# Kernel optimization log

Hardware: AMD Instinct MI355X
Metric: run time of the kernel (lower is better)

Reference implementation:

```python
import jax, jax.numpy as jnp
import numpy as np

B, N, F, T, K, O = 8, 1024, 64, 32, 3, 64


def setup_inputs() -> dict:
    key = jax.random.key(0)
    k0, k1, k2, k3 = jax.random.split(key, 4)
    x = jax.random.normal(k0, (B, N, F, T), dtype=jnp.float32)
    spatial_attention = jax.random.uniform(k1, (B, N, N), dtype=jnp.float32)
    cheb = jax.random.normal(k2, (K, N, N), dtype=jnp.float32) * 0.1  # stacked T_k
    Theta = jax.random.normal(k3, (K, F, O), dtype=jnp.float32) * (1.0 / np.sqrt(F))
    return {"x": x, "spatial_attention": spatial_attention, "cheb": cheb, "Theta": Theta}


def reference(x, spatial_attention, cheb, Theta):
    # Original per-timestep, per-k loop computes:
    #   rhs[b,i,f] = sum_j (T_k[j,i] * att[b,j,i])... note: T_k_with_at.permute(0,2,1) @ x
    #   i.e. rhs[b,i,f,t] = sum_j T_k[j,i]*att[b,j,i]*x[b,j,f,t]
    # Vectorized over all timesteps t and Chebyshev orders k at once.
    rhs = jnp.einsum('kji,bji,bjft->bkift', cheb, spatial_attention, x)  # (B,K,N,F,T)
    out = jnp.einsum('bkift,kfo->biot', rhs, Theta)                      # sum over k,f
    return jax.nn.relu(out)  # (B,N,O,T)
```

## Files before the change

### kernel.cpp

```cpp
#include <hip/hip_runtime.h>
#include <stdint.h>

#define Bn 8
#define Nn 1024
#define Fn 64
#define Tn 32
#define Kn 3
#define On 64
#define Rn (Kn * Nn)
#define Cn (On * Tn)
#define NT (Rn / 64)

typedef __bf16 bf16x8 __attribute__((ext_vector_type(8)));
typedef float f32x4 __attribute__((ext_vector_type(4)));
typedef __attribute__((address_space(1))) void gvoid;
typedef __attribute__((address_space(3))) void lvoid;

union BF8 { bf16x8 v; ushort s[8]; uint4 q; };

static __device__ __forceinline__ ushort f2bf(float f) {
  uint32_t u = __float_as_uint(f);
  return (ushort)((u + 0x7FFFu + ((u >> 16) & 1u)) >> 16);
}

static __device__ __forceinline__ void glds(const ushort* g, ushort* l) {
  __builtin_amdgcn_global_load_lds((gvoid*)g, (lvoid*)l, 16, 0, 0);
}

__global__ void k_thetaT(const float* __restrict__ Theta, ushort* __restrict__ ThT) {
  int idx = blockIdx.x * 256 + threadIdx.x;
  if (idx < Kn * On * Fn) {
    int k = idx / (On * Fn);
    int rem = idx % (On * Fn);
    int o = rem / Fn, f = rem % Fn;
    ThT[idx] = f2bf(Theta[(k * Fn + f) * On + o]);
  }
}

__global__ __launch_bounds__(256) void k_prepW(const float* __restrict__ att,
                                               const float* __restrict__ cheb,
                                               ushort* __restrict__ Wt) {
  __shared__ float tile[32][33];
  int i0 = blockIdx.x * 32, j0 = blockIdx.y * 32;
  int tid = threadIdx.x;
  int ci = tid & 31, rj = tid >> 5;
  float cv[4][Kn];
#pragma unroll
  for (int p = 0; p < 4; p++) {
    int j = j0 + rj + p * 8;
#pragma unroll
    for (int k = 0; k < Kn; k++)
      cv[p][k] = cheb[((size_t)k * Nn + j) * Nn + i0 + ci];
  }
  for (int b = 0; b < Bn; b++) {
    float av[4];
#pragma unroll
    for (int p = 0; p < 4; p++) {
      int j = j0 + rj + p * 8;
      av[p] = att[((size_t)b * Nn + j) * Nn + i0 + ci];
    }
    for (int k = 0; k < Kn; k++) {
#pragma unroll
      for (int p = 0; p < 4; p++)
        tile[rj + p * 8][ci] = av[p] * cv[p][k];
      __syncthreads();
#pragma unroll
      for (int p = 0; p < 4; p++) {
        int i = i0 + rj + p * 8;
        Wt[((size_t)b * Nn + i) * Rn + (size_t)k * Nn + j0 + ci] = f2bf(tile[ci][rj + p * 8]);
      }
      __syncthreads();
    }
  }
}

__global__ __launch_bounds__(512) void k_prepY(const float* __restrict__ x,
                                               const ushort* __restrict__ ThT,
                                               ushort* __restrict__ Yt) {
  __shared__ ushort ylds[1024 * 32];
  int jt = blockIdx.x, b = blockIdx.y;
  int j0 = jt * 32;
  int tid = threadIdx.x;
  int lane = tid & 63, w = tid >> 6;
  int l15 = lane & 15, l4 = lane >> 4;

  BF8 bfr[4][2][2];
#pragma unroll
  for (int jj = 0; jj < 4; jj++) {
    const float* xp = x + ((size_t)b * Nn + (j0 + w * 4 + jj)) * (Fn * Tn);
#pragma unroll
    for (int ks = 0; ks < 2; ks++)
#pragma unroll
      for (int tf = 0; tf < 2; tf++) {
        int t = tf * 16 + l15;
        int fb = ks * 32 + l4 * 8;
#pragma unroll
        for (int e = 0; e < 8; e++)
          bfr[jj][ks][tf].s[e] = f2bf(xp[(fb + e) * Tn + t]);
      }
  }

  for (int k = 0; k < Kn; k++) {
    for (int h = 0; h < 2; h++) {
      BF8 afr[2][2];
#pragma unroll
      for (int o2 = 0; o2 < 2; o2++)
#pragma unroll
        for (int ks = 0; ks < 2; ks++) {
          int o = h * 32 + o2 * 16 + l15;
          afr[o2][ks].q = *(const uint4*)&ThT[((size_t)k * On + o) * Fn + ks * 32 + l4 * 8];
        }
#pragma unroll
      for (int jj = 0; jj < 4; jj++) {
        f32x4 acc[2][2] = {};
#pragma unroll
        for (int ks = 0; ks < 2; ks++)
#pragma unroll
          for (int o2 = 0; o2 < 2; o2++)
#pragma unroll
            for (int tf = 0; tf < 2; tf++)
              acc[o2][tf] = __builtin_amdgcn_mfma_f32_16x16x32_bf16(
                  afr[o2][ks].v, bfr[jj][ks][tf].v, acc[o2][tf], 0, 0, 0);
#pragma unroll
        for (int o2 = 0; o2 < 2; o2++)
#pragma unroll
          for (int tf = 0; tf < 2; tf++)
#pragma unroll
            for (int q = 0; q < 4; q++) {
              int cl = (o2 * 16 + l4 * 4 + q) * Tn + tf * 16 + l15;
              ylds[cl * 32 + w * 4 + jj] = f2bf(acc[o2][tf][q]);
            }
      }
      __syncthreads();
      const uint32_t* yl32 = (const uint32_t*)ylds;
      uint32_t* Yt32 = (uint32_t*)Yt;
      int e = tid & 15, rowst = tid >> 4;
      for (int pass = 0; pass < 32; pass++) {
        int cl = pass * 32 + rowst;
        size_t off = ((size_t)b * Cn + (size_t)(h * 1024 + cl)) * Rn + (size_t)k * Nn + j0;
        Yt32[off / 2 + e] = yl32[cl * 16 + e];
      }
      __syncthreads();
    }
  }
}

__global__ __launch_bounds__(512, 2) void k_gemm(const ushort* __restrict__ Wt,
                                                 const ushort* __restrict__ Yt,
                                                 float* __restrict__ out) {
  extern __shared__ __align__(16) ushort smem[];
  ushort* As = smem;
  ushort* Bs = smem + 32768;

  int g = blockIdx.x;
  int b = g & 7, slot = g >> 3;
  int i0 = (slot & 3) * 256, c0 = (slot >> 2) * 256;
  int tid = threadIdx.x, lane = tid & 63, w = tid >> 6;
  int l15 = lane & 15, l4 = lane >> 4;
  int wm = w >> 2, wn = w & 3;

  const ushort* Ab = Wt + ((size_t)b * Nn + i0) * Rn;
  const ushort* Bb = Yt + ((size_t)b * Cn + c0) * Rn;

  int srcC = (((lane & 7) ^ (lane >> 3)) * 8);
  int arow0 = w * 8 + (lane >> 3);
  int brow0 = (w >> 2) * 64 + (w & 3) * 8 + (lane >> 3);

  int aL = (wm * 64 + l15) * 64;
  int bL = (wn * 32 + l15) * 64;
  int x7 = l15 & 7;
  int colx0 = ((l4) ^ x7) * 8;
  int colx1 = ((4 + l4) ^ x7) * 8;

  f32x4 acc[8][4] = {};
  BF8 afX[4][2], afY[4][2];
  BF8 bfX[2][2], bfY[2][2];

#define MFMA_(a_, b_, c_) __builtin_amdgcn_mfma_f32_16x16x32_bf16((a_), (b_), (c_), 0, 0, 0)
#define BAR() asm volatile("s_barrier" ::: "memory")
#define PRIO1 __builtin_amdgcn_s_setprio(1)
#define PRIO0 __builtin_amdgcn_s_setprio(0)
#define VMC(n_) asm volatile("s_waitcnt vmcnt(" #n_ ")" ::: "memory")

#define STAGE_A(t_, h_) { int bo_ = ((t_) & 1) * 16384 + (h_) * 8192 + w * 512; \
    const ushort* gp_ = Ab + (size_t)(arow0 + (h_) * 64) * Rn + (t_) * 64 + srcC; \
    glds(gp_, As + bo_); \
    glds(gp_ + 128 * (size_t)Rn, As + bo_ + 4096); }
#define STAGE_B(t_, h_) { int bo_ = ((t_) & 1) * 16384 + (h_) * 8192 + w * 512; \
    const ushort* gp_ = Bb + (size_t)(brow0 + (h_) * 32) * Rn + (t_) * 64 + srcC; \
    glds(gp_, Bs + bo_); \
    glds(gp_ + 128 * (size_t)Rn, Bs + bo_ + 4096); }

#define RD_A(DST_, bo_, mh_) { _Pragma("unroll") for (int m = 0; m < 4; m++) { \
    int ba_ = (bo_) + (mh_) * 8192 + aL + m * 1024; \
    DST_[m][0].q = *(const uint4*)&As[ba_ + colx0]; \
    DST_[m][1].q = *(const uint4*)&As[ba_ + colx1]; } }
#define RD_B(DST_, bo_, nh_) { _Pragma("unroll") for (int n = 0; n < 2; n++) { \
    int bb_ = (bo_) + (nh_) * 8192 + bL + n * 1024; \
    DST_[n][0].q = *(const uint4*)&Bs[bb_ + colx0]; \
    DST_[n][1].q = *(const uint4*)&Bs[bb_ + colx1]; } }

#define MMC(AF_, BF_, MO_, NO_) { _Pragma("unroll") for (int ks = 0; ks < 2; ks++) \
    _Pragma("unroll") for (int m = 0; m < 4; m++) \
      _Pragma("unroll") for (int n = 0; n < 2; n++) \
        acc[(MO_) + m][(NO_) + n] = MFMA_(AF_[m][ks].v, BF_[n][ks].v, acc[(MO_) + m][(NO_) + n]); }

  STAGE_A(0, 0); STAGE_B(0, 0); STAGE_B(0, 1); STAGE_A(0, 1); STAGE_A(1, 0);
  VMC(6); BAR();
  RD_A(afX, 0, 0); RD_B(bfX, 0, 0);

#define TILE(t_, S0_, S1_, S2_, W0_, W1_, W3_, LAST_) { \
    int bo_c = ((t_) & 1) * 16384; \
    VMC(W0_); BAR(); \
    RD_B(bfY, bo_c, 1); \
    if (S0_) STAGE_B((t_) + 1, 0); \
    PRIO1; MMC(afX, bfX, 0, 0); PRIO0; \
    VMC(W1_); BAR(); \
    RD_A(afY, bo_c, 1); \
    if (S1_) { STAGE_B((t_) + 1, 1); STAGE_A((t_) + 1, 1); } \
    PRIO1; MMC(afX, bfY, 0, 2); PRIO0; \
    if (S2_) STAGE_A((t_) + 2, 0); \
    PRIO1; MMC(afY, bfX, 4, 0); PRIO0; \
    if (!(LAST_)) { VMC(W3_); BAR(); \
      RD_A(afX, bo_c ^ 16384, 0); RD_B(bfX, bo_c ^ 16384, 0); } \
    PRIO1; MMC(afY, bfY, 4, 2); PRIO0; \
  }

  for (int t = 0; t < NT - 2; ++t)
    TILE(t, 1, 1, 1, 4, 4, 6, 0);
  TILE(NT - 2, 1, 1, 0, 4, 4, 4, 0);
  TILE(NT - 1, 0, 0, 0, 2, 0, 0, 1);

#undef TILE
#undef MMC
#undef RD_B
#undef RD_A
#undef STAGE_B
#undef STAGE_A
#undef VMC

  float* ob = out + (size_t)b * Nn * Cn;
#pragma unroll
  for (int m = 0; m < 8; m++) {
    int i = i0 + wm * 128 + m * 16 + l4 * 4;
#pragma unroll
    for (int n = 0; n < 4; n++) {
      int c = c0 + wn * 64 + n * 16 + l15;
#pragma unroll
      for (int q = 0; q < 4; q++)
        ob[(size_t)(i + q) * Cn + c] = fmaxf(acc[m][n][q], 0.0f);
    }
  }
}

extern "C" void kernel_launch(void* const* d_in, const int* in_sizes, int n_in,
                              void* d_out, int out_size, void* d_ws, size_t ws_size,
                              hipStream_t stream) {
  const float* x     = (const float*)d_in[0];
  const float* att   = (const float*)d_in[1];
  const float* cheb  = (const float*)d_in[2];
  const float* Theta = (const float*)d_in[3];
  float* out = (float*)d_out;

  char* ws = (char*)d_ws;
  ushort* ThT = (ushort*)ws;
  ushort* Wt  = (ushort*)(ws + 65536);
  ushort* Yt  = (ushort*)(ws + 65536 + 50331648ull);

  hipFuncSetAttribute((const void*)k_gemm, hipFuncAttributeMaxDynamicSharedMemorySize, 131072);

  k_thetaT<<<48, 256, 0, stream>>>(Theta, ThT);
  k_prepW<<<dim3(32, 32), 256, 0, stream>>>(att, cheb, Wt);
  k_prepY<<<dim3(32, 8), 512, 0, stream>>>(x, ThT, Yt);
  k_gemm<<<256, 512, 131072, stream>>>(Wt, Yt, out);
}
```

Measured before the change: 155.6 us.

## Restructure GEMM main loop to prefetch full tile two steps ahead

The prologue now loads both halves of A and B for the first two K-tiles before entering the loop. Each loop iteration now issues all global-to-LDS loads for tile t+2, spread across the four MFMA quarters, and uses different vmcnt waits. Next-tile fragment reads from LDS are interleaved between the MFMA blocks so compute overlaps the loads. The aim is to hide global memory latency behind more MFMA work. The cost is more outstanding loads and a more delicate barrier and wait ordering on the double-buffered LDS.

```diff
diff --git a/kernel.cpp b/kernel.cpp
--- a/kernel.cpp
+++ b/kernel.cpp
@@ -205,31 +205,37 @@
       _Pragma("unroll") for (int n = 0; n < 2; n++) \
         acc[(MO_) + m][(NO_) + n] = MFMA_(AF_[m][ks].v, BF_[n][ks].v, acc[(MO_) + m][(NO_) + n]); }
 
-  STAGE_A(0, 0); STAGE_B(0, 0); STAGE_B(0, 1); STAGE_A(0, 1); STAGE_A(1, 0);
-  VMC(6); BAR();
+  STAGE_A(0, 0); STAGE_B(0, 0); STAGE_B(0, 1); STAGE_A(0, 1);
+  STAGE_A(1, 0); STAGE_B(1, 0); STAGE_B(1, 1); STAGE_A(1, 1);
+  VMC(8); BAR();
   RD_A(afX, 0, 0); RD_B(bfX, 0, 0);
 
-#define TILE(t_, S0_, S1_, S2_, W0_, W1_, W3_, LAST_) { \
-    int bo_c = ((t_) & 1) * 16384; \
-    VMC(W0_); BAR(); \
-    RD_B(bfY, bo_c, 1); \
-    if (S0_) STAGE_B((t_) + 1, 0); \
+#define TILE(t_, S2_, W1_, W2_, LAST_) { \
+    int cur = ((t_) & 1) * 16384, nxt = cur ^ 16384; \
+     \
+    RD_B(bfY, cur, 1); \
     PRIO1; MMC(afX, bfX, 0, 0); PRIO0; \
+     \
     VMC(W1_); BAR(); \
-    RD_A(afY, bo_c, 1); \
-    if (S1_) { STAGE_B((t_) + 1, 1); STAGE_A((t_) + 1, 1); } \
+    RD_A(afY, cur, 1); \
+    if (S2_) STAGE_A((t_) + 2, 0); \
     PRIO1; MMC(afX, bfY, 0, 2); PRIO0; \
-    if (S2_) STAGE_A((t_) + 2, 0); \
+    if (!(LAST_)) RD_A(afX, nxt, 0); \
+     \
+    VMC(W2_); BAR(); \
+    if (S2_) { STAGE_B((t_) + 2, 0); STAGE_B((t_) + 2, 1); } \
     PRIO1; MMC(afY, bfX, 4, 0); PRIO0; \
-    if (!(LAST_)) { VMC(W3_); BAR(); \
-      RD_A(afX, bo_c ^ 16384, 0); RD_B(bfX, bo_c ^ 16384, 0); } \
+    if (!(LAST_)) RD_B(bfX, nxt, 0); \
+     \
+    BAR(); \
+    if (S2_) STAGE_A((t_) + 2, 1); \
     PRIO1; MMC(afY, bfY, 4, 2); PRIO0; \
   }
 
   for (int t = 0; t < NT - 2; ++t)
-    TILE(t, 1, 1, 1, 4, 4, 6, 0);
-  TILE(NT - 2, 1, 1, 0, 4, 4, 4, 0);
-  TILE(NT - 1, 0, 0, 0, 2, 0, 0, 1);
+    TILE(t, 1, 6, 4, 0);
+  TILE(NT - 2, 0, 6, 2, 0);
+  TILE(NT - 1, 0, 0, 0, 1);
 
 #undef TILE
 #undef MMC
```

Result: slower. 174.0 us (+11.8%).

## Load GEMM B operand directly from global into registers, drop B LDS staging

Applied to the files above, without the earlier changes.

The B tile (Yt) is no longer staged through LDS; each lane loads its MFMA B fragments straight from global memory into registers, while A keeps the double-buffered LDS path. The pipeline is rewritten as a simpler loop with full vmcnt(0) waits, and dynamic shared memory is halved. This removes LDS traffic and barriers for B, at the cost of duplicated global reads across the waves sharing the same columns and coarser wait synchronisation that can expose latency.

```diff
diff --git a/kernel.cpp b/kernel.cpp
--- a/kernel.cpp
+++ b/kernel.cpp
@@ -150,7 +150,6 @@
                                                  float* __restrict__ out) {
   extern __shared__ __align__(16) ushort smem[];
   ushort* As = smem;
-  ushort* Bs = smem + 32768;
 
   int g = blockIdx.x;
   int b = g & 7, slot = g >> 3;
@@ -164,13 +163,13 @@
 
   int srcC = (((lane & 7) ^ (lane >> 3)) * 8);
   int arow0 = w * 8 + (lane >> 3);
-  int brow0 = (w >> 2) * 64 + (w & 3) * 8 + (lane >> 3);
 
   int aL = (wm * 64 + l15) * 64;
-  int bL = (wn * 32 + l15) * 64;
   int x7 = l15 & 7;
   int colx0 = ((l4) ^ x7) * 8;
   int colx1 = ((4 + l4) ^ x7) * 8;
+
+  const ushort* bG = Bb + (size_t)(wn * 64 + l15) * Rn + l4 * 8;
 
   f32x4 acc[8][4] = {};
   BF8 afX[4][2], afY[4][2];
@@ -180,64 +179,62 @@
 #define BAR() asm volatile("s_barrier" ::: "memory")
 #define PRIO1 __builtin_amdgcn_s_setprio(1)
 #define PRIO0 __builtin_amdgcn_s_setprio(0)
-#define VMC(n_) asm volatile("s_waitcnt vmcnt(" #n_ ")" ::: "memory")
+#define VMC0() asm volatile("s_waitcnt vmcnt(0)" ::: "memory")
 
 #define STAGE_A(t_, h_) { int bo_ = ((t_) & 1) * 16384 + (h_) * 8192 + w * 512; \
     const ushort* gp_ = Ab + (size_t)(arow0 + (h_) * 64) * Rn + (t_) * 64 + srcC; \
     glds(gp_, As + bo_); \
     glds(gp_ + 128 * (size_t)Rn, As + bo_ + 4096); }
-#define STAGE_B(t_, h_) { int bo_ = ((t_) & 1) * 16384 + (h_) * 8192 + w * 512; \
-    const ushort* gp_ = Bb + (size_t)(brow0 + (h_) * 32) * Rn + (t_) * 64 + srcC; \
-    glds(gp_, Bs + bo_); \
-    glds(gp_ + 128 * (size_t)Rn, Bs + bo_ + 4096); }
 
 #define RD_A(DST_, bo_, mh_) { _Pragma("unroll") for (int m = 0; m < 4; m++) { \
     int ba_ = (bo_) + (mh_) * 8192 + aL + m * 1024; \
     DST_[m][0].q = *(const uint4*)&As[ba_ + colx0]; \
     DST_[m][1].q = *(const uint4*)&As[ba_ + colx1]; } }
-#define RD_B(DST_, bo_, nh_) { _Pragma("unroll") for (int n = 0; n < 2; n++) { \
-    int bb_ = (bo_) + (nh_) * 8192 + bL + n * 1024; \
-    DST_[n][0].q = *(const uint4*)&Bs[bb_ + colx0]; \
-    DST_[n][1].q = *(const uint4*)&Bs[bb_ + colx1]; } }
-
-#define MMC(AF_, BF_, MO_, NO_) { _Pragma("unroll") for (int ks = 0; ks < 2; ks++) \
+
+#define B_LOAD(DST_, nh_, t_) { _Pragma("unroll") for (int nn = 0; nn < 2; nn++) \
+    _Pragma("unroll") for (int ks = 0; ks < 2; ks++) \
+      DST_[nn][ks].q = *(const uint4*)(bG + (size_t)((nh_) * 32 + nn * 16) * Rn + (t_) * 64 + ks * 32); }
+
+#define MMC(AF_, BF_, MO_, NO_) { PRIO1; _Pragma("unroll") for (int ks = 0; ks < 2; ks++) \
     _Pragma("unroll") for (int m = 0; m < 4; m++) \
       _Pragma("unroll") for (int n = 0; n < 2; n++) \
-        acc[(MO_) + m][(NO_) + n] = MFMA_(AF_[m][ks].v, BF_[n][ks].v, acc[(MO_) + m][(NO_) + n]); }
-
-  STAGE_A(0, 0); STAGE_B(0, 0); STAGE_B(0, 1); STAGE_A(0, 1); STAGE_A(1, 0);
-  VMC(6); BAR();
-  RD_A(afX, 0, 0); RD_B(bfX, 0, 0);
-
-#define TILE(t_, S0_, S1_, S2_, W0_, W1_, W3_, LAST_) { \
-    int bo_c = ((t_) & 1) * 16384; \
-    VMC(W0_); BAR(); \
-    RD_B(bfY, bo_c, 1); \
-    if (S0_) STAGE_B((t_) + 1, 0); \
-    PRIO1; MMC(afX, bfX, 0, 0); PRIO0; \
-    VMC(W1_); BAR(); \
-    RD_A(afY, bo_c, 1); \
-    if (S1_) { STAGE_B((t_) + 1, 1); STAGE_A((t_) + 1, 1); } \
-    PRIO1; MMC(afX, bfY, 0, 2); PRIO0; \
-    if (S2_) STAGE_A((t_) + 2, 0); \
-    PRIO1; MMC(afY, bfX, 4, 0); PRIO0; \
-    if (!(LAST_)) { VMC(W3_); BAR(); \
-      RD_A(afX, bo_c ^ 16384, 0); RD_B(bfX, bo_c ^ 16384, 0); } \
-    PRIO1; MMC(afY, bfY, 4, 2); PRIO0; \
-  }
-
-  for (int t = 0; t < NT - 2; ++t)
-    TILE(t, 1, 1, 1, 4, 4, 6, 0);
-  TILE(NT - 2, 1, 1, 0, 4, 4, 4, 0);
-  TILE(NT - 1, 0, 0, 0, 2, 0, 0, 1);
-
-#undef TILE
+        acc[(MO_) + m][(NO_) + n] = MFMA_(AF_[m][ks].v, BF_[n][ks].v, acc[(MO_) + m][(NO_) + n]); \
+    PRIO0; }
+
+  STAGE_A(0, 0); STAGE_A(0, 1); STAGE_A(1, 0); STAGE_A(1, 1);
+  B_LOAD(bfX, 0, 0);
+  VMC0(); BAR();
+  RD_A(afX, 0, 0);
+
+  for (int t = 0; t < NT - 1; ++t) {
+    int cur = (t & 1) * 16384, nxt = cur ^ 16384;
+    RD_A(afY, cur, 1);
+    STAGE_A(t + 1, 0);
+    B_LOAD(bfY, 1, t);
+    MMC(afX, bfX, 0, 0);
+    STAGE_A(t + 1, 1);
+    MMC(afY, bfX, 4, 0);
+    B_LOAD(bfX, 0, t + 1);
+    MMC(afX, bfY, 0, 2);
+    VMC0(); BAR();
+    RD_A(afX, nxt, 0);
+    MMC(afY, bfY, 4, 2);
+  }
+  {
+    int cur = ((NT - 1) & 1) * 16384;
+    RD_A(afY, cur, 1);
+    B_LOAD(bfY, 1, NT - 1);
+    MMC(afX, bfX, 0, 0);
+    MMC(afY, bfX, 4, 0);
+    MMC(afX, bfY, 0, 2);
+    MMC(afY, bfY, 4, 2);
+  }
+
 #undef MMC
-#undef RD_B
+#undef B_LOAD
 #undef RD_A
-#undef STAGE_B
 #undef STAGE_A
-#undef VMC
+#undef VMC0
 
   float* ob = out + (size_t)b * Nn * Cn;
 #pragma unroll
@@ -267,10 +264,10 @@
   ushort* Wt  = (ushort*)(ws + 65536);
   ushort* Yt  = (ushort*)(ws + 65536 + 50331648ull);
 
-  hipFuncSetAttribute((const void*)k_gemm, hipFuncAttributeMaxDynamicSharedMemorySize, 131072);
+  hipFuncSetAttribute((const void*)k_gemm, hipFuncAttributeMaxDynamicSharedMemorySize, 65536);
 
   k_thetaT<<<48, 256, 0, stream>>>(Theta, ThT);
   k_prepW<<<dim3(32, 32), 256, 0, stream>>>(att, cheb, Wt);
   k_prepY<<<dim3(32, 8), 512, 0, stream>>>(x, ThT, Yt);
-  k_gemm<<<256, 512, 131072, stream>>>(Wt, Yt, out);
-}
+  k_gemm<<<256, 512, 65536, stream>>>(Wt, Yt, out);
+}
```

Measured after the change: 210.2 us. 1.35x slower.
